# Kernel tuning notes

Hardware: AMD Instinct MI355X
Metric: run time of the kernel (lower is better)

Reference implementation:

```python
import jax, jax.numpy as jnp
import numpy as np

N_ATOMS = 100          # n_atoms from init_kwargs
BATCH = 1024           # dataset / batch size (single-batch usage per docstring)


def setup_inputs() -> dict:
    key = jax.random.key(0)
    k1, k2 = jax.random.split(key)
    # descriptors = pairwise distances between atoms -> 6 nonzero derivs per desc per frame
    ii, jj = np.triu_indices(N_ATOMS, 1)               # [D] each
    D = ii.shape[0]                                    # 4950 descriptors
    atoms = np.stack([ii, jj], axis=1)                 # [D, 2]
    atom_pd = np.repeat(atoms, 3, axis=1).reshape(-1)  # [D*6]: i,i,i,j,j,j per desc
    dim_pd = np.tile(np.array([0, 1, 2, 0, 1, 2]), D)  # [D*6]
    des_pd = np.repeat(np.arange(D), 6)                # [D*6]

    batch_ind = np.repeat(np.arange(BATCH), D * 6)     # [nnz]
    des_ind = np.tile(des_pd, BATCH)                   # [nnz]
    atom_ind = np.tile(atom_pd, BATCH)                 # [nnz]
    dim_ind = np.tile(dim_pd, BATCH)                   # [nnz]
    # faithful shifted index: per-frame offset + atom*3 + dim
    scatter_idx = batch_ind * (N_ATOMS * 3) + atom_ind * 3 + dim_ind

    nnz = batch_ind.shape[0]
    x = jax.random.normal(k1, (BATCH, D), dtype=jnp.float32)      # dq/d(descriptors)
    left = jax.random.normal(k2, (nnz,), dtype=jnp.float32)       # nonzero d(desc)/d(pos)
    return {
        "x": x,
        "left": left,
        "batch_ind": jnp.asarray(batch_ind, jnp.int32),
        "des_ind": jnp.asarray(des_ind, jnp.int32),
        "scatter_idx": jnp.asarray(scatter_idx, jnp.int32),
    }


def reference(x, left, batch_ind, des_ind, scatter_idx):
    # gather right operand: dq/d(desc) for each nonzero left entry
    right = x[batch_ind, des_ind]                      # [nnz]
    src = left * right                                 # chain rule terms
    # scatter-add into (frame, atom, dim) bins, then square (square modulus comps)
    acc = jax.ops.segment_sum(src, scatter_idx, num_segments=BATCH * N_ATOMS * 3)
    return (acc * acc).reshape(BATCH, N_ATOMS * 3)
```

## Files before the change

### kernel.cpp

```cpp
#include <hip/hip_runtime.h>


#define N_ATOMS 100
#define D_DESC  4950
#define BATCH   1024
#define NOUT    300

#define SZ4_MAX 3728

__device__ __forceinline__ int rowstart(int i) { return (i * (199 - i)) >> 1; }

__global__ __launch_bounds__(1024, 8)
void sd_partial_kernel(const float* __restrict__ x,
                       const float* __restrict__ left,
                       float* __restrict__ ws) {
    __shared__ float4 sz4[SZ4_MAX];
    __shared__ float  spart[NOUT][8];

    const int b   = blockIdx.x >> 1;
    const int sub = blockIdx.x & 1;
    const int tid = threadIdx.x;

    const int f4start = sub ? 3697 : 0;
    const int f4cnt   = sub ? 3728 : 3698;
    const int zb      = f4start * 4;
    const int r0      = sub ? 29 : 0;
    const int r1      = sub ? 99 : 29;

    for (int t = tid; t < NOUT * 8; t += 1024) ((float*)spart)[t] = 0.0f;

    const float4* __restrict__ lb4 =
        (const float4*)(left + (size_t)b * (D_DESC * 6)) + f4start;
    const float* __restrict__ xb = x + (size_t)b * D_DESC;

    #pragma unroll
    for (int k = 0; k < 4; ++k) {
        const int idx = tid + k * 1024;
        if (idx < f4cnt) {
            const float4 L = lb4[idx];
            const int g  = (f4start + idx) * 4;
            const int d0 = g / 6;
            const int r  = g - 6 * d0;
            const float x0 = xb[d0];
            const float x1 = xb[(g + 3) / 6];
            float4 z;
            z.x = L.x * x0;
            z.y = L.y * x0;
            z.z = L.z * ((r + 2 >= 6) ? x1 : x0);
            z.w = L.w * ((r + 3 >= 6) ? x1 : x0);
            sz4[idx] = z;
        }
    }
    __syncthreads();

    const float* __restrict__ sz = (const float*)sz4;
    const int nr = r1 - r0;

    if (tid < 3 * nr) {
        const int a  = r0 + tid / 3;
        const int q  = tid - 3 * (tid / 3);
        const int rs = rowstart(a);
        const int len = 99 - a;
        const float* __restrict__ base = sz + (rs * 6 - zb);
        float s0 = 0.f, s1 = 0.f, s2 = 0.f;
        for (int m = q; m < len; m += 3) {
            const float2 c01 = *(const float2*)(base + m * 6);
            const float  c2  = base[m * 6 + 2];
            s0 += c01.x; s1 += c01.y; s2 += c2;
        }
        spart[a * 3 + 0][q] = s0;
        spart[a * 3 + 1][q] = s1;
        spart[a * 3 + 2][q] = s2;
    }

    const int cbase = 3 * nr;
    const int nc    = sub ? 70 : 99;
    const int j0    = sub ? 30 : 1;
    const int t2    = tid - cbase;
    if (t2 >= 0 && t2 < 3 * nc) {
        const int j = j0 + t2 / 3;
        const int q = t2 - 3 * (t2 / 3);
        float s3 = 0.f, s4 = 0.f, s5 = 0.f;
        int i = r0 + q;
        const int iend = (j < r1) ? j : r1;
        if (i < iend) {
            int d    = rowstart(i) + j - i - 1;
            int step = 291 - 3 * i;
            while (true) {
                const int f = d * 6 + 3 - zb;
                s3 += sz[f]; s4 += sz[f + 1]; s5 += sz[f + 2];
                i += 3;
                if (i >= iend) break;
                d += step; step -= 9;
            }
        }
        spart[j * 3 + 0][3 + q] = s3;
        spart[j * 3 + 1][3 + q] = s4;
        spart[j * 3 + 2][3 + q] = s5;
    }
    __syncthreads();

    if (tid < NOUT) {
        const float* p = spart[tid];
        ws[((size_t)sub * BATCH + b) * NOUT + tid] =
            p[0] + p[1] + p[2] + p[3] + p[4] + p[5];
    }
}

__global__ __launch_bounds__(256)
void sd_combine_kernel(const float* __restrict__ ws, float* __restrict__ out) {
    const int idx = blockIdx.x * 256 + threadIdx.x;
    const float4 u = ((const float4*)ws)[idx];
    const float4 v = ((const float4*)(ws + (size_t)BATCH * NOUT))[idx];
    float4 o;
    o.x = u.x + v.x; o.x *= o.x;
    o.y = u.y + v.y; o.y *= o.y;
    o.z = u.z + v.z; o.z *= o.z;
    o.w = u.w + v.w; o.w *= o.w;
    ((float4*)out)[idx] = o;
}

extern "C" void kernel_launch(void* const* d_in, const int* in_sizes, int n_in,
                              void* d_out, int out_size, void* d_ws, size_t ws_size,
                              hipStream_t stream) {
    const float* x    = (const float*)d_in[0];
    const float* left = (const float*)d_in[1];
    float* ws  = (float*)d_ws;
    float* out = (float*)d_out;

    sd_partial_kernel<<<BATCH * 2, 1024, 0, stream>>>(x, left, ws);
    sd_combine_kernel<<<(BATCH * NOUT / 4) / 256, 256, 0, stream>>>(ws, out);
}
```

Measured before the change: 332.5 us.

## Split each frame into four row-chunk blocks of 512 threads

Each batch frame is now split into four blocks covering balanced row ranges, read from constant tables, instead of two 1024-thread blocks. The goal is smaller blocks and less shared memory per block, so more blocks can be resident per CU and the load of the left array overlaps better. The combine kernel now sums four partial workspaces, which doubles workspace traffic and adds partial-sum writes. The column-sum pass also runs over all columns after r0 in each chunk, so some threads do little work.

Measured after the change: 334.8 us. Within noise of the previous version (+0.7%).

```diff
diff --git a/kernel.cpp b/kernel.cpp
--- a/kernel.cpp
+++ b/kernel.cpp
@@ -5,29 +5,33 @@
 #define D_DESC  4950
 #define BATCH   1024
 #define NOUT    300
+#define SZ4_MAX 1964
 
-#define SZ4_MAX 3728
+__constant__ int c_r0[4]  = {0, 14, 31, 53};
+__constant__ int c_r1[4]  = {14, 31, 53, 99};
+__constant__ int c_f40[4] = {0, 1942, 3906, 5803};
+__constant__ int c_f41[4] = {1943, 3906, 5804, 7425};
 
 __device__ __forceinline__ int rowstart(int i) { return (i * (199 - i)) >> 1; }
 
-__global__ __launch_bounds__(1024, 8)
+__global__ __launch_bounds__(512, 8)
 void sd_partial_kernel(const float* __restrict__ x,
                        const float* __restrict__ left,
                        float* __restrict__ ws) {
     __shared__ float4 sz4[SZ4_MAX];
-    __shared__ float  spart[NOUT][8];
+    __shared__ float  spart[NOUT][6];
 
-    const int b   = blockIdx.x >> 1;
-    const int sub = blockIdx.x & 1;
-    const int tid = threadIdx.x;
+    const int b     = blockIdx.x >> 2;
+    const int chunk = blockIdx.x & 3;
+    const int tid   = threadIdx.x;
 
-    const int f4start = sub ? 3697 : 0;
-    const int f4cnt   = sub ? 3728 : 3698;
+    const int r0      = c_r0[chunk];
+    const int r1      = c_r1[chunk];
+    const int f4start = c_f40[chunk];
+    const int f4cnt   = c_f41[chunk] - f4start;
     const int zb      = f4start * 4;
-    const int r0      = sub ? 29 : 0;
-    const int r1      = sub ? 99 : 29;
 
-    for (int t = tid; t < NOUT * 8; t += 1024) ((float*)spart)[t] = 0.0f;
+    for (int t = tid; t < NOUT * 6; t += 512) ((float*)spart)[t] = 0.0f;
 
     const float4* __restrict__ lb4 =
         (const float4*)(left + (size_t)b * (D_DESC * 6)) + f4start;
@@ -35,7 +39,7 @@
 
     #pragma unroll
     for (int k = 0; k < 4; ++k) {
-        const int idx = tid + k * 1024;
+        const int idx = tid + k * 512;
         if (idx < f4cnt) {
             const float4 L = lb4[idx];
             const int g  = (f4start + idx) * 4;
@@ -57,9 +61,9 @@
     const int nr = r1 - r0;
 
     if (tid < 3 * nr) {
-        const int a  = r0 + tid / 3;
-        const int q  = tid - 3 * (tid / 3);
-        const int rs = rowstart(a);
+        const int a   = r0 + tid / 3;
+        const int q   = tid - 3 * (tid / 3);
+        const int rs  = rowstart(a);
         const int len = 99 - a;
         const float* __restrict__ base = sz + (rs * 6 - zb);
         float s0 = 0.f, s1 = 0.f, s2 = 0.f;
@@ -74,11 +78,10 @@
     }
 
     const int cbase = 3 * nr;
-    const int nc    = sub ? 70 : 99;
-    const int j0    = sub ? 30 : 1;
+    const int nc    = 99 - r0;
     const int t2    = tid - cbase;
     if (t2 >= 0 && t2 < 3 * nc) {
-        const int j = j0 + t2 / 3;
+        const int j = r0 + 1 + t2 / 3;
         const int q = t2 - 3 * (t2 / 3);
         float s3 = 0.f, s4 = 0.f, s5 = 0.f;
         int i = r0 + q;
@@ -102,7 +105,7 @@
 
     if (tid < NOUT) {
         const float* p = spart[tid];
-        ws[((size_t)sub * BATCH + b) * NOUT + tid] =
+        ws[((size_t)chunk * BATCH + b) * NOUT + tid] =
             p[0] + p[1] + p[2] + p[3] + p[4] + p[5];
     }
 }
@@ -110,13 +113,16 @@
 __global__ __launch_bounds__(256)
 void sd_combine_kernel(const float* __restrict__ ws, float* __restrict__ out) {
     const int idx = blockIdx.x * 256 + threadIdx.x;
-    const float4 u = ((const float4*)ws)[idx];
-    const float4 v = ((const float4*)(ws + (size_t)BATCH * NOUT))[idx];
+    const size_t stride = (size_t)BATCH * NOUT;
+    const float4 u0 = ((const float4*)ws)[idx];
+    const float4 u1 = ((const float4*)(ws + stride))[idx];
+    const float4 u2 = ((const float4*)(ws + 2 * stride))[idx];
+    const float4 u3 = ((const float4*)(ws + 3 * stride))[idx];
     float4 o;
-    o.x = u.x + v.x; o.x *= o.x;
-    o.y = u.y + v.y; o.y *= o.y;
-    o.z = u.z + v.z; o.z *= o.z;
-    o.w = u.w + v.w; o.w *= o.w;
+    o.x = u0.x + u1.x + u2.x + u3.x; o.x *= o.x;
+    o.y = u0.y + u1.y + u2.y + u3.y; o.y *= o.y;
+    o.z = u0.z + u1.z + u2.z + u3.z; o.z *= o.z;
+    o.w = u0.w + u1.w + u2.w + u3.w; o.w *= o.w;
     ((float4*)out)[idx] = o;
 }
 
@@ -128,6 +134,6 @@
     float* ws  = (float*)d_ws;
     float* out = (float*)d_out;
 
-    sd_partial_kernel<<<BATCH * 2, 1024, 0, stream>>>(x, left, ws);
+    sd_partial_kernel<<<BATCH * 4, 512, 0, stream>>>(x, left, ws);
     sd_combine_kernel<<<(BATCH * NOUT / 4) / 256, 256, 0, stream>>>(ws, out);
 }
```
